# Kernel tuning notes

Hardware: AMD Instinct MI355X
Metric: run time of the kernel (lower is better)

## Reference

```python
import jax, jax.numpy as jnp
import numpy as np

K = 3          # kernel size (both dims)
PAD = 1        # padding used both for offset_mask conv and deform_conv2d
KK = K * K


def setup_inputs() -> dict:
    key = jax.random.key(0)
    k0, k1, k2, k3, k4 = jax.random.split(key, 5)
    B, C, H, W, O = 8, 64, 64, 64, 64
    input_feat = jax.random.normal(k0, (B, C, H, W), jnp.float32)
    degrad_inter = jax.random.normal(k1, (B, C, H, W), jnp.float32)
    stdv = 1.0 / np.sqrt(C * K * K)
    weight = jax.random.uniform(k2, (O, C, K, K), jnp.float32, -stdv, stdv)
    # small-magnitude offset/mask conv params -> realistic small learned offsets
    om_weight = jax.random.normal(k3, (3 * KK, 2 * C, K, K), jnp.float32) * 0.01
    om_bias = jax.random.normal(k4, (3 * KK,), jnp.float32) * 0.01
    return {"input_feat": input_feat, "degrad_inter": degrad_inter,
            "weight": weight, "om_weight": om_weight, "om_bias": om_bias}


def _conv2d(x, w, b):
    out = jax.lax.conv_general_dilated(
        x, w, window_strides=(1, 1), padding=((PAD, PAD), (PAD, PAD)),
        dimension_numbers=("NCHW", "OIHW", "NCHW"))
    return out + b[None, :, None, None]


def _deform_conv2d(x, offset, mask, weight):
    # x: (B,C,H,W); offset: (B,2*KK,H,W) with channel 2k=dy_k, 2k+1=dx_k;
    # mask: (B,KK,H,W); weight: (O,C,K,K). stride=1, padding=PAD, dilation=1.
    B, C, H, W = x.shape
    O = weight.shape[0]
    off = offset.reshape(B, KK, 2, H, W)
    dy, dx = off[:, :, 0], off[:, :, 1]                       # (B,KK,H,W)

    ky, kx = jnp.meshgrid(jnp.arange(K), jnp.arange(K), indexing="ij")
    ky = ky.reshape(KK).astype(x.dtype)
    kx = kx.reshape(KK).astype(x.dtype)
    hh = jnp.arange(H, dtype=x.dtype)
    ww = jnp.arange(W, dtype=x.dtype)
    # absolute fractional sample locations: (B,KK,H,W)
    y = hh[None, None, :, None] - PAD + ky[None, :, None, None] + dy
    xq = ww[None, None, None, :] - PAD + kx[None, :, None, None] + dx

    y0 = jnp.floor(y).astype(jnp.int32)
    x0 = jnp.floor(xq).astype(jnp.int32)
    y1, x1 = y0 + 1, x0 + 1
    wy = y - y0.astype(x.dtype)
    wx = xq - x0.astype(x.dtype)

    x_flat = x.reshape(B, C, H * W)

    def gather(yi, xi):
        valid = (yi >= 0) & (yi < H) & (xi >= 0) & (xi < W)
        idx = jnp.clip(yi, 0, H - 1) * W + jnp.clip(xi, 0, W - 1)  # (B,KK,H,W)
        vals = jax.vmap(lambda im, ix: im[:, ix])(x_flat, idx)     # (B,C,KK,H,W)
        return vals * valid[:, None].astype(x.dtype)

    wy_ = wy[:, None]  # (B,1,KK,H,W)
    wx_ = wx[:, None]
    sampled = (gather(y0, x0) * (1 - wy_) * (1 - wx_)
               + gather(y0, x1) * (1 - wy_) * wx_
               + gather(y1, x0) * wy_ * (1 - wx_)
               + gather(y1, x1) * wy_ * wx_)                       # (B,C,KK,H,W)
    sampled = sampled * mask[:, None]
    return jnp.einsum("bckhw,ock->bohw", sampled, weight.reshape(O, C, KK))


def reference(input_feat, degrad_inter, weight, om_weight, om_bias):
    concat = jnp.concatenate([input_feat, degrad_inter], axis=1)
    om = _conv2d(concat, om_weight, om_bias)                       # (B,3*KK,H,W)
    off1, off2, mask = jnp.split(om, 3, axis=1)
    offset = jnp.concatenate([off1, off2], axis=1)                 # (B,2*KK,H,W)
    mask = jax.nn.sigmoid(mask)                                    # (B,KK,H,W)
    return _deform_conv2d(input_feat, offset, mask, weight)
```

## Files before the change

kernel.cpp:

```cpp
#include <hip/hip_runtime.h>
#include <math.h>

#define WO_PK_OFF 36864
#define CATT_OFF  73728

typedef short  short8  __attribute__((ext_vector_type(8)));
typedef float  float4v __attribute__((ext_vector_type(4)));
typedef unsigned int uint4v __attribute__((ext_vector_type(4)));

static __device__ __forceinline__ short f2bf(float f) {
    unsigned int u = __builtin_bit_cast(unsigned int, f);
    u += 0x7FFFu + ((u >> 16) & 1u);
    return (short)(u >> 16);
}
static __device__ __forceinline__ float bf2f(unsigned short u) {
    return __builtin_bit_cast(float, (unsigned int)u << 16);
}
static __device__ __forceinline__ unsigned int cvt_pk_bf16(float lo, float hi) {
    unsigned int r;
    asm("v_cvt_pk_bf16_f32 %0, %1, %2" : "=v"(r) : "v"(lo), "v"(hi));
    return r;
}

__global__ __launch_bounds__(256) void prep_kernel(
    const float* __restrict__ feat, const float* __restrict__ deg,
    unsigned short* __restrict__ catT,
    const float* __restrict__ weight, const float* __restrict__ om_weight,
    short* __restrict__ wd_pk, short* __restrict__ wo_pk)
{
    __shared__ unsigned short T[64 * 136];
    const int tid = threadIdx.x;

    if (blockIdx.x >= 512) {
        int idx = (blockIdx.x - 512) * 256 + tid;
        if (idx < 36864) {
            int j = idx & 7, o = (idx >> 3) & 63, lq = (idx >> 9) & 3, ks = idx >> 11;
            int t = ks >> 1, c = (ks & 1) * 32 + lq * 8 + j;
            wd_pk[idx] = f2bf(weight[(o * 64 + c) * 9 + t]);
        } else {
            int e = idx - 36864;
            int j = e & 7, oc = (e >> 3) & 31, lq = (e >> 8) & 3, ks2 = e >> 10;
            int quarter = ks2 / 9, t = ks2 - quarter * 9;
            int cg = quarter * 32 + lq * 8 + j;
            wo_pk[e] = (oc < 27) ? f2bf(om_weight[(oc * 128 + cg) * 9 + t])
                                 : (short)0;
        }
        return;
    }

    const int b = blockIdx.x >> 6, h = blockIdx.x & 63;
    const int lane = tid & 63, wv = tid >> 6;
#pragma unroll
    for (int cc = 0; cc < 32; cc++) {
        int c = wv * 32 + cc;
        const float* src = (c < 64)
            ? (feat + (size_t)(b * 64 + c) * 4096)
            : (deg  + (size_t)(b * 64 + (c - 64)) * 4096);
        T[lane * 136 + c] = (unsigned short)f2bf(src[h * 64 + lane]);
    }
    __syncthreads();
    const int px = tid >> 2, seg = tid & 3;
    unsigned short* dst = catT + (size_t)(b * 4096 + h * 64 + px) * 128 + seg * 32;
#pragma unroll
    for (int j = 0; j < 4; j++)
        *(uint4*)(dst + j * 8) = *(const uint4*)&T[px * 136 + seg * 32 + j * 8];
}

__global__ __launch_bounds__(256) void fused_kernel(
    const unsigned short* __restrict__ catT, const short* __restrict__ wd_pk,
    const short* __restrict__ wo_pk, const float* __restrict__ om_bias,
    float* __restrict__ out)
{
    __shared__ __align__(16) short lwd[36864];
    __shared__ __align__(16) float Tsm[4 * 448];
    const int tid = threadIdx.x;
    const int lane = tid & 63, wv = tid >> 6;
    const int l16 = lane & 15, lq = lane >> 4;
    const int gw = blockIdx.x * 4 + wv;
    const int b = gw >> 8, tile = gw & 255;
    const int h = tile >> 2, w0 = (tile & 3) << 4;
    const int pxx = w0 + l16;
    const unsigned short* cb = catT + (size_t)b * 4096 * 128;

    {
        const uint4* src = (const uint4*)wd_pk;
        uint4* dst = (uint4*)lwd;
#pragma unroll
        for (int i = 0; i < 18; i++)
            dst[i * 256 + tid] = src[i * 256 + tid];
    }

    float4v oacc0 = {0.f, 0.f, 0.f, 0.f};
    float4v oacc1 = {0.f, 0.f, 0.f, 0.f};
    const short8 zf = {0, 0, 0, 0, 0, 0, 0, 0};
#pragma unroll
    for (int quarter = 0; quarter < 4; quarter++) {
#pragma unroll
        for (int t = 0; t < 9; t++) {
            const int ky = t / 3, kx = t - ky * 3;
            const int yy = h - 1 + ky;
            if (yy >= 0 && yy <= 63) {
                int xx = pxx - 1 + kx;
                bool okx = (xx >= 0) & (xx <= 63);
                int xc = min(max(xx, 0), 63);
                short8 bfr = *(const short8*)(cb + (yy * 64 + xc) * 128
                                                 + quarter * 32 + lq * 8);
                bfr = okx ? bfr : zf;
                const short8* Ap = (const short8*)(wo_pk
                    + (size_t)((quarter * 9 + t) * 4 + lq) * 256);
                oacc0 = __builtin_amdgcn_mfma_f32_16x16x32_bf16(
                    Ap[l16], bfr, oacc0, 0, 0, 0);
                oacc1 = __builtin_amdgcn_mfma_f32_16x16x32_bf16(
                    Ap[16 + l16], bfr, oacc1, 0, 0, 0);
            }
        }
    }

    float* Tw = Tsm + wv * 448;
#pragma unroll
    for (int r = 0; r < 4; r++) {
        Tw[l16 * 28 + lq * 4 + r] = oacc0[r];
        if (lq < 3)
            Tw[l16 * 28 + 16 + lq * 4 + r] = oacc1[r];
    }
    __syncthreads();
    float omv[28];
#pragma unroll
    for (int jj = 0; jj < 7; jj++)
        *(float4v*)&omv[jj * 4] = *(const float4v*)&Tw[l16 * 28 + jj * 4];
#pragma unroll
    for (int j = 0; j < 27; j++) omv[j] += om_bias[j];

    float4v acc[4];
#pragma unroll
    for (int mt = 0; mt < 4; mt++) acc[mt] = (float4v){0.f, 0.f, 0.f, 0.f};
#pragma unroll
    for (int t = 0; t < 9; t++) {
        const int ky = t / 3, kx = t - ky * 3;
        float dy = omv[2 * t], dx = omv[2 * t + 1];
        float mm = 1.f / (1.f + __expf(-omv[18 + t]));
        float yf = (float)(h - 1 + ky) + dy;
        float xf = (float)(pxx - 1 + kx) + dx;
        float fy = floorf(yf), fx = floorf(xf);
        int y0 = (int)fy, x0 = (int)fx;
        float wy = yf - fy, wx = xf - fx;
        bool vy0 = (y0 >= 0) & (y0 < 64);
        bool vy1 = (y0 >= -1) & (y0 < 63);
        bool vx0 = (x0 >= 0) & (x0 < 64);
        bool vx1 = (x0 >= -1) & (x0 < 63);
        float a0 = (1.f - wy) * mm, a1 = wy * mm;
        float W00 = a0 * (1.f - wx) * (float)(vy0 & vx0);
        float W01 = a0 * wx         * (float)(vy0 & vx1);
        float W10 = a1 * (1.f - wx) * (float)(vy1 & vx0);
        float W11 = a1 * wx         * (float)(vy1 & vx1);
        int iy0 = min(max(y0, 0), 63),     ix0 = min(max(x0, 0), 63);
        int iy1 = min(max(y0 + 1, 0), 63), ix1 = min(max(x0 + 1, 0), 63);
        int O00 = (iy0 * 64 + ix0) * 128, O01 = (iy0 * 64 + ix1) * 128;
        int O10 = (iy1 * 64 + ix0) * 128, O11 = (iy1 * 64 + ix1) * 128;
#pragma unroll
        for (int qh = 0; qh < 2; qh++) {
            const int cho = qh * 32 + lq * 8;
            uint4v u00 = *(const uint4v*)(cb + O00 + cho);
            uint4v u01 = *(const uint4v*)(cb + O01 + cho);
            uint4v u10 = *(const uint4v*)(cb + O10 + cho);
            uint4v u11 = *(const uint4v*)(cb + O11 + cho);
            uint4v br;
#pragma unroll
            for (int p = 0; p < 4; p++) {
                float l00 = __builtin_bit_cast(float, u00[p] << 16);
                float h00 = __builtin_bit_cast(float, u00[p] & 0xffff0000u);
                float l01 = __builtin_bit_cast(float, u01[p] << 16);
                float h01 = __builtin_bit_cast(float, u01[p] & 0xffff0000u);
                float l10 = __builtin_bit_cast(float, u10[p] << 16);
                float h10 = __builtin_bit_cast(float, u10[p] & 0xffff0000u);
                float l11 = __builtin_bit_cast(float, u11[p] << 16);
                float h11 = __builtin_bit_cast(float, u11[p] & 0xffff0000u);
                float slo = W00 * l00 + W01 * l01 + W10 * l10 + W11 * l11;
                float shi = W00 * h00 + W01 * h01 + W10 * h10 + W11 * h11;
                br[p] = cvt_pk_bf16(slo, shi);
            }
            short8 bfr = __builtin_bit_cast(short8, br);
            const short8* Dp = (const short8*)(lwd
                + (size_t)((t * 2 + qh) * 4 + lq) * 512);
            acc[0] = __builtin_amdgcn_mfma_f32_16x16x32_bf16(
                Dp[l16], bfr, acc[0], 0, 0, 0);
            acc[1] = __builtin_amdgcn_mfma_f32_16x16x32_bf16(
                Dp[16 + l16], bfr, acc[1], 0, 0, 0);
            acc[2] = __builtin_amdgcn_mfma_f32_16x16x32_bf16(
                Dp[32 + l16], bfr, acc[2], 0, 0, 0);
            acc[3] = __builtin_amdgcn_mfma_f32_16x16x32_bf16(
                Dp[48 + l16], bfr, acc[3], 0, 0, 0);
        }
    }

    float* ob = out + (size_t)(b * 64) * 4096 + h * 64 + w0 + l16;
#pragma unroll
    for (int mt = 0; mt < 4; mt++)
#pragma unroll
        for (int r = 0; r < 4; r++)
            ob[(mt * 16 + lq * 4 + r) * 4096] = acc[mt][r];
}

extern "C" void kernel_launch(void* const* d_in, const int* in_sizes, int n_in,
                              void* d_out, int out_size, void* d_ws, size_t ws_size,
                              hipStream_t stream)
{
    const float* feat      = (const float*)d_in[0];
    const float* deg       = (const float*)d_in[1];
    const float* weight    = (const float*)d_in[2];
    const float* om_weight = (const float*)d_in[3];
    const float* om_bias   = (const float*)d_in[4];
    float* out = (float*)d_out;
    short* wss = (short*)d_ws;
    unsigned short* catT = (unsigned short*)(wss + CATT_OFF);

    hipLaunchKernelGGL(prep_kernel, dim3(800), dim3(256), 0, stream,
                       feat, deg, catT, weight, om_weight,
                       wss, wss + WO_PK_OFF);
    hipLaunchKernelGGL(fused_kernel, dim3(512), dim3(256), 0, stream,
                       catT, wss, wss + WO_PK_OFF, om_bias, out);
}
```

Measured before the change: 116.1 us.

## Software-pipeline deformable gather loads and reorder offset conv loop by tap

The deformable sampling loop now issues the bilinear-corner loads for the next tap while the current tap is being interpolated and multiplied, a double-buffered prefetch meant to hide global memory latency. The offset conv loop is reordered to loop over taps first and load all four channel quarters at once. Out-of-range x now reads from a zeroed padding region appended to the workspace instead of using a select. Launch bounds request two blocks per CU, which caps registers while the prefetch buffers raise register demand, so spilling is a risk.

```diff
diff --git a/kernel.cpp b/kernel.cpp
--- a/kernel.cpp
+++ b/kernel.cpp
@@ -3,6 +3,7 @@
 
 #define WO_PK_OFF 36864
 #define CATT_OFF  73728
+#define ZR_OFF    4268032
 
 typedef short  short8  __attribute__((ext_vector_type(8)));
 typedef float  float4v __attribute__((ext_vector_type(4)));
@@ -12,9 +13,6 @@
     unsigned int u = __builtin_bit_cast(unsigned int, f);
     u += 0x7FFFu + ((u >> 16) & 1u);
     return (short)(u >> 16);
-}
-static __device__ __forceinline__ float bf2f(unsigned short u) {
-    return __builtin_bit_cast(float, (unsigned int)u << 16);
 }
 static __device__ __forceinline__ unsigned int cvt_pk_bf16(float lo, float hi) {
     unsigned int r;
@@ -37,13 +35,15 @@
             int j = idx & 7, o = (idx >> 3) & 63, lq = (idx >> 9) & 3, ks = idx >> 11;
             int t = ks >> 1, c = (ks & 1) * 32 + lq * 8 + j;
             wd_pk[idx] = f2bf(weight[(o * 64 + c) * 9 + t]);
-        } else {
+        } else if (idx < 73728) {
             int e = idx - 36864;
             int j = e & 7, oc = (e >> 3) & 31, lq = (e >> 8) & 3, ks2 = e >> 10;
             int quarter = ks2 / 9, t = ks2 - quarter * 9;
             int cg = quarter * 32 + lq * 8 + j;
             wo_pk[e] = (oc < 27) ? f2bf(om_weight[(oc * 128 + cg) * 9 + t])
                                  : (short)0;
+        } else if (idx < 73856) {
+            wd_pk[ZR_OFF + (idx - 73728)] = 0;
         }
         return;
     }
@@ -66,7 +66,7 @@
         *(uint4*)(dst + j * 8) = *(const uint4*)&T[px * 136 + seg * 32 + j * 8];
 }
 
-__global__ __launch_bounds__(256) void fused_kernel(
+__global__ __launch_bounds__(256, 2) void fused_kernel(
     const unsigned short* __restrict__ catT, const short* __restrict__ wd_pk,
     const short* __restrict__ wo_pk, const float* __restrict__ om_bias,
     float* __restrict__ out)
@@ -81,6 +81,7 @@
     const int h = tile >> 2, w0 = (tile & 3) << 4;
     const int pxx = w0 + l16;
     const unsigned short* cb = catT + (size_t)b * 4096 * 128;
+    const unsigned short* zbase = catT + (size_t)4194304;
 
     {
         const uint4* src = (const uint4*)wd_pk;
@@ -92,20 +93,24 @@
 
     float4v oacc0 = {0.f, 0.f, 0.f, 0.f};
     float4v oacc1 = {0.f, 0.f, 0.f, 0.f};
-    const short8 zf = {0, 0, 0, 0, 0, 0, 0, 0};
-#pragma unroll
-    for (int quarter = 0; quarter < 4; quarter++) {
-#pragma unroll
-        for (int t = 0; t < 9; t++) {
-            const int ky = t / 3, kx = t - ky * 3;
-            const int yy = h - 1 + ky;
-            if (yy >= 0 && yy <= 63) {
-                int xx = pxx - 1 + kx;
-                bool okx = (xx >= 0) & (xx <= 63);
-                int xc = min(max(xx, 0), 63);
-                short8 bfr = *(const short8*)(cb + (yy * 64 + xc) * 128
-                                                 + quarter * 32 + lq * 8);
-                bfr = okx ? bfr : zf;
+#pragma unroll
+    for (int t = 0; t < 9; t++) {
+        const int ky = t / 3, kx = t - ky * 3;
+        const int yy = h - 1 + ky;
+        if (yy >= 0 && yy <= 63) {
+            int xx = pxx - 1 + kx;
+            bool okx = (xx >= 0) & (xx <= 63);
+            const unsigned short* pl = okx
+                ? (cb + (yy * 64 + xx) * 128 + lq * 8)
+                : (zbase + lq * 8);
+            short8 bq0 = *(const short8*)(pl);
+            short8 bq1 = *(const short8*)(pl + 32);
+            short8 bq2 = *(const short8*)(pl + 64);
+            short8 bq3 = *(const short8*)(pl + 96);
+#pragma unroll
+            for (int quarter = 0; quarter < 4; quarter++) {
+                short8 bfr = quarter == 0 ? bq0 : quarter == 1 ? bq1
+                           : quarter == 2 ? bq2 : bq3;
                 const short8* Ap = (const short8*)(wo_pk
                     + (size_t)((quarter * 9 + t) * 4 + lq) * 256);
                 oacc0 = __builtin_amdgcn_mfma_f32_16x16x32_bf16(
@@ -134,8 +139,11 @@
     float4v acc[4];
 #pragma unroll
     for (int mt = 0; mt < 4; mt++) acc[mt] = (float4v){0.f, 0.f, 0.f, 0.f};
-#pragma unroll
-    for (int t = 0; t < 9; t++) {
+
+    float  Wt[2][4];
+    uint4v u0[2][4], u1[2][4];
+
+    auto prep_tap = [&](int t, int s) {
         const int ky = t / 3, kx = t - ky * 3;
         float dy = omv[2 * t], dx = omv[2 * t + 1];
         float mm = 1.f / (1.f + __expf(-omv[18 + t]));
@@ -149,21 +157,38 @@
         bool vx0 = (x0 >= 0) & (x0 < 64);
         bool vx1 = (x0 >= -1) & (x0 < 63);
         float a0 = (1.f - wy) * mm, a1 = wy * mm;
-        float W00 = a0 * (1.f - wx) * (float)(vy0 & vx0);
-        float W01 = a0 * wx         * (float)(vy0 & vx1);
-        float W10 = a1 * (1.f - wx) * (float)(vy1 & vx0);
-        float W11 = a1 * wx         * (float)(vy1 & vx1);
+        Wt[s][0] = a0 * (1.f - wx) * (float)(vy0 & vx0);
+        Wt[s][1] = a0 * wx         * (float)(vy0 & vx1);
+        Wt[s][2] = a1 * (1.f - wx) * (float)(vy1 & vx0);
+        Wt[s][3] = a1 * wx         * (float)(vy1 & vx1);
         int iy0 = min(max(y0, 0), 63),     ix0 = min(max(x0, 0), 63);
         int iy1 = min(max(y0 + 1, 0), 63), ix1 = min(max(x0 + 1, 0), 63);
         int O00 = (iy0 * 64 + ix0) * 128, O01 = (iy0 * 64 + ix1) * 128;
         int O10 = (iy1 * 64 + ix0) * 128, O11 = (iy1 * 64 + ix1) * 128;
+        const int c0 = lq * 8, c1 = 32 + lq * 8;
+        u0[s][0] = *(const uint4v*)(cb + O00 + c0);
+        u0[s][1] = *(const uint4v*)(cb + O01 + c0);
+        u0[s][2] = *(const uint4v*)(cb + O10 + c0);
+        u0[s][3] = *(const uint4v*)(cb + O11 + c0);
+        u1[s][0] = *(const uint4v*)(cb + O00 + c1);
+        u1[s][1] = *(const uint4v*)(cb + O01 + c1);
+        u1[s][2] = *(const uint4v*)(cb + O10 + c1);
+        u1[s][3] = *(const uint4v*)(cb + O11 + c1);
+    };
+
+    prep_tap(0, 0);
+#pragma unroll
+    for (int t = 0; t < 9; t++) {
+        const int s = t & 1;
+        if (t < 8) prep_tap(t + 1, s ^ 1);
+        const float W00 = Wt[s][0], W01 = Wt[s][1];
+        const float W10 = Wt[s][2], W11 = Wt[s][3];
 #pragma unroll
         for (int qh = 0; qh < 2; qh++) {
-            const int cho = qh * 32 + lq * 8;
-            uint4v u00 = *(const uint4v*)(cb + O00 + cho);
-            uint4v u01 = *(const uint4v*)(cb + O01 + cho);
-            uint4v u10 = *(const uint4v*)(cb + O10 + cho);
-            uint4v u11 = *(const uint4v*)(cb + O11 + cho);
+            uint4v u00 = qh ? u1[s][0] : u0[s][0];
+            uint4v u01 = qh ? u1[s][1] : u0[s][1];
+            uint4v u10 = qh ? u1[s][2] : u0[s][2];
+            uint4v u11 = qh ? u1[s][3] : u0[s][3];
             uint4v br;
 #pragma unroll
             for (int p = 0; p < 4; p++) {
@@ -214,7 +239,7 @@
     short* wss = (short*)d_ws;
     unsigned short* catT = (unsigned short*)(wss + CATT_OFF);
 
-    hipLaunchKernelGGL(prep_kernel, dim3(800), dim3(256), 0, stream,
+    hipLaunchKernelGGL(prep_kernel, dim3(801), dim3(256), 0, stream,
                        feat, deg, catT, weight, om_weight,
                        wss, wss + WO_PK_OFF);
     hipLaunchKernelGGL(fused_kernel, dim3(512), dim3(256), 0, stream,
```

Result: no change. 114.7 us (-1.2%).
